# Kernel tuning notes

Measured on AMD Instinct MI355X. Metric: run time of the kernel, lower is better.

## Reference

```python
import jax, jax.numpy as jnp
import numpy as np

N = 100000        # num nodes
E = 1600000       # num edges
IN_DIM = 256
HID = 64          # per-head out_dim
OUT_DIM = 256
H = 4             # num heads
EDGE_DIM = 16
NEG_SLOPE = 0.2

def _xavier(key, shape):
    fan_in, fan_out = shape[-2], shape[-1]
    bound = float(np.sqrt(6.0 / (fan_in + fan_out)))
    return jax.random.uniform(key, shape, jnp.float32, -bound, bound)

def setup_inputs() -> dict:
    key = jax.random.key(0)
    ks = jax.random.split(key, 8)
    x = jax.random.normal(ks[0], (N, IN_DIM), jnp.float32)
    edge_index = jax.random.randint(ks[1], (2, E), 0, N, jnp.int64)
    edge_attr = jax.random.normal(ks[2], (E, EDGE_DIM), jnp.float32)
    W = _xavier(ks[3], (H, IN_DIM, HID))
    W_edge = _xavier(ks[4], (H, EDGE_DIM, HID))
    att = _xavier(ks[5], (H, 3 * HID, 1))[..., 0]          # [H, 3*HID]
    proj_w = _xavier(ks[6], (H * HID, OUT_DIM))
    proj_b = jnp.zeros((OUT_DIM,), jnp.float32)
    return {"x": x, "edge_index": edge_index, "edge_attr": edge_attr,
            "W": W, "W_edge": W_edge, "att": att,
            "proj_w": proj_w, "proj_b": proj_b}

def reference(x, edge_index, edge_attr, W, W_edge, att, proj_w, proj_b):
    src = edge_index[0]  # x_j (source) indices
    dst = edge_index[1]  # x_i (target) indices; softmax/aggregation segments

    # Per-head node transform: [H, N, HID]
    xw = jnp.einsum('ni,hio->hno', x, W)
    x_i = xw[:, dst]                                  # [H, E, HID]
    x_j = xw[:, src]                                  # [H, E, HID]
    edge_proj = jnp.einsum('ed,hdo->heo', edge_attr, W_edge)  # [H, E, HID]

    a1, a2, a3 = att[:, :HID], att[:, HID:2*HID], att[:, 2*HID:]  # [H, HID] each
    e = (jnp.einsum('heo,ho->he', x_i, a1)
         + jnp.einsum('heo,ho->he', x_j, a2)
         + jnp.einsum('heo,ho->he', edge_proj, a3))   # [H, E]
    e = jnp.where(e >= 0, e, NEG_SLOPE * e)           # LeakyReLU

    def seg_softmax(eh):  # eh: [E]
        m = jax.ops.segment_max(eh, dst, num_segments=N)
        m = jnp.where(jnp.isfinite(m), m, 0.0)
        ex = jnp.exp(eh - m[dst])
        s = jax.ops.segment_sum(ex, dst, num_segments=N)
        return ex / (s[dst] + 1e-16)

    alpha = jax.vmap(seg_softmax)(e)                  # [H, E]  (dropout: eval mode)

    msg = x_j * alpha[..., None]                      # [H, E, HID]
    out_h = jax.vmap(lambda m: jax.ops.segment_sum(m, dst, num_segments=N))(msg)  # [H, N, HID]
    out = jnp.transpose(out_h, (1, 0, 2)).reshape(N, H * HID)  # concat heads
    out = out @ proj_w + proj_b
    return jax.nn.elu(out)
```

## Files before the change

### kernel.cpp

```cpp
#include <hip/hip_runtime.h>
#include <hip/hip_bf16.h>
#include <stdint.h>

#define N_NODES 100000
#define E_EDGES 1600000
#define NEG_SLOPE 0.2f
#define NBUCK 1563
#define BK_SH 6
#define CAP 1536

typedef short short8 __attribute__((ext_vector_type(8)));
typedef float f32x4 __attribute__((ext_vector_type(4)));

__device__ __forceinline__ unsigned short f2bf(float f) {
  union { float f; unsigned int u; } c; c.f = f;
  unsigned int u = c.u;
  unsigned int r = u + 0x7FFFu + ((u >> 16) & 1u);
  return (unsigned short)(r >> 16);
}
__device__ __forceinline__ float asf(unsigned int u) {
  union { unsigned int u; float f; } c; c.u = u;
  return c.f;
}

__global__ void k_detect(const void* ei, int* flag) {
  int t = threadIdx.x;
  int v = ((const int*)ei)[2 * t + 1];
  unsigned long long b = __ballot(v != 0);
  if (t == 0) *flag = (b != 0ull) ? 1 : 0;
}

__global__ void k_prep(const float* __restrict__ W, const float* __restrict__ proj_w,
                       const float* __restrict__ W_edge, const float* __restrict__ att,
                       unsigned short* __restrict__ Bt, unsigned short* __restrict__ Pt,
                       float* __restrict__ w3) {
  int t = blockIdx.x * 256 + threadIdx.x;
  if (t < 65536) {
    int col = t >> 8, k = t & 255;
    int h = col >> 6, o = col & 63;
    Bt[t] = f2bf(W[h * 16384 + k * 64 + o]);
  } else if (t < 131072) {
    int t2 = t - 65536;
    int o = t2 >> 8, i = t2 & 255;
    int orig = (i >> 6) * 64 + ((i >> 2) & 15) + 16 * (i & 3);
    Pt[t2] = f2bf(proj_w[orig * 256 + o]);
  } else if (t < 131136) {
    int t3 = t - 131072;
    int h = t3 >> 4, d = t3 & 15;
    float s = 0.f;
    for (int o = 0; o < 64; ++o)
      s += W_edge[h * 1024 + d * 64 + o] * att[h * 192 + 128 + o];
    w3[t3] = s;
  }
}

__global__ __launch_bounds__(256, 4) void k_gemm_x(const float* __restrict__ x,
    const unsigned short* __restrict__ Bt, const float* __restrict__ att,
    unsigned int* __restrict__ xwq, float* __restrict__ scl4,
    float* __restrict__ s1, float* __restrict__ s2) {
  __shared__ unsigned short As[16384];
  const int bm = blockIdx.x * 64;
  const int t = threadIdx.x;

#pragma unroll
  for (int i = 0; i < 16; ++i) {
    int c = i * 256 + t;
    int row = c >> 6, f4 = c & 63;
    uint2 w = make_uint2(0u, 0u);
    if (bm + row < N_NODES) {
      float4 v = *(const float4*)(x + (size_t)(bm + row) * 256 + f4 * 4);
      w.x = (unsigned int)f2bf(v.x) | ((unsigned int)f2bf(v.y) << 16);
      w.y = (unsigned int)f2bf(v.z) | ((unsigned int)f2bf(v.w) << 16);
    }
    int phys = row * 512 + (((f4 >> 1) ^ (row & 7)) << 4) + ((f4 & 1) << 3);
    *(uint2*)((char*)As + phys) = w;
  }
  __syncthreads();

  const int wave = t >> 6;
  const int lane = t & 63;
  const int l16 = lane & 15, lg = lane >> 4;
  const int colbase = wave * 64;
  f32x4 acc[4][4];
#pragma unroll
  for (int i = 0; i < 4; i++)
#pragma unroll
    for (int j = 0; j < 4; j++) acc[i][j] = (f32x4){0.f, 0.f, 0.f, 0.f};

  short8 bcur[4], bnxt[4];
#pragma unroll
  for (int ni = 0; ni < 4; ni++)
    bcur[ni] = *(const short8*)(Bt + (colbase + ni * 16 + l16) * 256 + lg * 8);

#pragma unroll
  for (int ks = 0; ks < 8; ++ks) {
    short8 a[4];
#pragma unroll
    for (int mi = 0; mi < 4; mi++) {
      int row = mi * 16 + l16;
      int phys = row * 512 + (((ks * 4 + lg) ^ (row & 7)) << 4);
      a[mi] = *(const short8*)((const char*)As + phys);
    }
    if (ks < 7) {
      const int k0n = (ks + 1) * 32 + lg * 8;
#pragma unroll
      for (int ni = 0; ni < 4; ni++)
        bnxt[ni] = *(const short8*)(Bt + (colbase + ni * 16 + l16) * 256 + k0n);
    }
#pragma unroll
    for (int mi = 0; mi < 4; mi++)
#pragma unroll
      for (int ni = 0; ni < 4; ni++)
        acc[mi][ni] = __builtin_amdgcn_mfma_f32_16x16x32_bf16(a[mi], bcur[ni], acc[mi][ni], 0, 0, 0);
#pragma unroll
    for (int ni = 0; ni < 4; ni++) bcur[ni] = bnxt[ni];
  }

  float a1v[4], a2v[4];
#pragma unroll
  for (int ni = 0; ni < 4; ni++) {
    a1v[ni] = att[wave * 192 + ni * 16 + l16];
    a2v[ni] = att[wave * 192 + 64 + ni * 16 + l16];
  }
#pragma unroll
  for (int mi = 0; mi < 4; mi++) {
#pragma unroll
    for (int r = 0; r < 4; r++) {
      int row = bm + mi * 16 + lg * 4 + r;
      float a0 = acc[mi][0][r], a1 = acc[mi][1][r], a2 = acc[mi][2][r], a3 = acc[mi][3][r];
      float p1 = a0 * a1v[0] + a1 * a1v[1] + a2 * a1v[2] + a3 * a1v[3];
      float p2 = a0 * a2v[0] + a1 * a2v[1] + a2 * a2v[2] + a3 * a2v[3];
      float mx = fmaxf(fmaxf(fabsf(a0), fabsf(a1)), fmaxf(fabsf(a2), fabsf(a3)));
#pragma unroll
      for (int m = 1; m < 16; m <<= 1) {
        p1 += __shfl_xor(p1, m, 64);
        p2 += __shfl_xor(p2, m, 64);
        mx = fmaxf(mx, __shfl_xor(mx, m, 64));
      }
      if (row < N_NODES) {
        mx += 1e-30f;
        float inv = 127.f / mx;
        int q0 = __float2int_rn(a0 * inv);
        int q1 = __float2int_rn(a1 * inv);
        int q2 = __float2int_rn(a2 * inv);
        int q3 = __float2int_rn(a3 * inv);
        unsigned int pk = (q0 & 0xFF) | ((q1 & 0xFF) << 8) | ((q2 & 0xFF) << 16) |
                          ((unsigned int)(q3 & 0xFF) << 24);
        xwq[(size_t)row * 64 + wave * 16 + l16] = pk;
        if (l16 == 0) {
          s1[row * 4 + wave] = p1;
          s2[row * 4 + wave] = p2;
          scl4[row * 4 + wave] = mx * (1.f / 127.f);
        }
      }
    }
  }
}

__global__ __launch_bounds__(1024) void k_hist(const void* ei, const int* __restrict__ flag,
                                               int* __restrict__ bhist) {
  __shared__ int h[NBUCK];
  for (int i = threadIdx.x; i < NBUCK; i += 1024) h[i] = 0;
  __syncthreads();
  int f = *flag;
  int base = blockIdx.x * 4096;
#pragma unroll
  for (int k = 0; k < 4; ++k) {
    int e = base + k * 1024 + threadIdx.x;
    if (e < E_EDGES) {
      int dst = f ? ((const int*)ei)[E_EDGES + e] : (int)(((const long long*)ei)[E_EDGES + e]);
      atomicAdd(&h[dst >> BK_SH], 1);
    }
  }
  __syncthreads();
  for (int i = threadIdx.x; i < NBUCK; i += 1024) {
    int c = h[i];
    if (c) atomicAdd(&bhist[i], c);
  }
}

__global__ __launch_bounds__(1024) void k_scanb(const int* __restrict__ bhist,
                                                int* __restrict__ boff, int* __restrict__ bcur) {
  __shared__ int s[2048];
  int t = threadIdx.x;
  int ia = t, ib = t + 1024;
  int va = (ia < NBUCK) ? bhist[ia] : 0;
  int vb = (ib < NBUCK) ? bhist[ib] : 0;
  s[ia] = va; s[ib] = vb;
  __syncthreads();
  for (int off = 1; off < 2048; off <<= 1) {
    int xa = (ia >= off) ? s[ia - off] : 0;
    int xb = (ib >= off) ? s[ib - off] : 0;
    __syncthreads();
    s[ia] += xa; s[ib] += xb;
    __syncthreads();
  }
  if (ia < NBUCK) { boff[ia] = s[ia] - va; bcur[ia] = s[ia] - va; }
  if (ib < NBUCK) { boff[ib] = s[ib] - vb; bcur[ib] = s[ib] - vb; }
  if (t == 0) boff[NBUCK] = E_EDGES;
}

__global__ __launch_bounds__(1024) void k_edge(const void* ei, const int* __restrict__ flag,
                       const float* __restrict__ edge_attr,
                       const float* __restrict__ s1, const float* __restrict__ s2,
                       const float* __restrict__ w3g, int* __restrict__ bcur,
                       uint4* __restrict__ evs) {
  __shared__ float w3[64];
  __shared__ int cnt[NBUCK];
  __shared__ int rb[NBUCK];
  __shared__ int cur[NBUCK];
  const int t = threadIdx.x;
  for (int i = t; i < NBUCK; i += 1024) { cnt[i] = 0; cur[i] = 0; }
  if (t < 64) w3[t] = w3g[t];
  __syncthreads();

  const int f = *flag;
  const int base = blockIdx.x * 4096;
  int dstv[4], srcv[4];
  unsigned int pav[4], pbv[4];
#pragma unroll
  for (int k = 0; k < 4; ++k) {
    int e = base + k * 1024 + t;
    dstv[k] = -1;
    if (e < E_EDGES) {
      int src, dst;
      if (f) {
        src = ((const int*)ei)[e];
        dst = ((const int*)ei)[E_EDGES + e];
      } else {
        src = (int)(((const long long*)ei)[e]);
        dst = (int)(((const long long*)ei)[E_EDGES + e]);
      }
      float4 sd = *(const float4*)(s1 + (size_t)dst * 4);
      float4 ss = *(const float4*)(s2 + (size_t)src * 4);
      float ea[16];
#pragma unroll
      for (int i = 0; i < 4; i++) {
        float4 v = *(const float4*)(edge_attr + (size_t)e * 16 + i * 4);
        ea[4 * i] = v.x; ea[4 * i + 1] = v.y; ea[4 * i + 2] = v.z; ea[4 * i + 3] = v.w;
      }
      float ex[4];
#pragma unroll
      for (int h = 0; h < 4; h++) {
        float d = 0.f;
#pragma unroll
        for (int i = 0; i < 16; i++) d += ea[i] * w3[h * 16 + i];
        float v = (&sd.x)[h] + (&ss.x)[h] + d;
        v = (v >= 0.f) ? v : NEG_SLOPE * v;
        ex[h] = __expf(v);
      }
      dstv[k] = dst;
      srcv[k] = src;
      pav[k] = ((unsigned int)f2bf(ex[1]) << 16) | (unsigned int)f2bf(ex[0]);
      pbv[k] = ((unsigned int)f2bf(ex[3]) << 16) | (unsigned int)f2bf(ex[2]);
      atomicAdd(&cnt[dst >> BK_SH], 1);
    }
  }
  __syncthreads();
  for (int i = t; i < NBUCK; i += 1024) {
    int c = cnt[i];
    if (c) rb[i] = atomicAdd(&bcur[i], c);
  }
  __syncthreads();
#pragma unroll
  for (int k = 0; k < 4; ++k) {
    if (dstv[k] >= 0) {
      int bk = dstv[k] >> BK_SH;
      int pos = rb[bk] + atomicAdd(&cur[bk], 1);
      evs[pos] = make_uint4((unsigned int)srcv[k], pav[k], pbv[k],
                            (unsigned int)(dstv[k] & 63));
    }
  }
}

__global__ __launch_bounds__(256) void k_aggr(const int* __restrict__ boff,
    const uint4* __restrict__ evs, const unsigned int* __restrict__ xwq,
    const float* __restrict__ scl4, unsigned short* __restrict__ out_hb) {
  __shared__ int lsrc[CAP];
  __shared__ uint2 lw[CAP];
  __shared__ int cnt[64], bs[64], cur[64];
  const int b = blockIdx.x;
  const int t = threadIdx.x;
  const int e0 = boff[b];
  const int ne = boff[b + 1] - e0;
  if (t < 64) { cnt[t] = 0; cur[t] = 0; }
  __syncthreads();
  const bool ok = (ne <= CAP);
  if (ok) {
    uint4 rv[6];
#pragma unroll
    for (int k = 0; k < 6; ++k) {
      int i = k * 256 + t;
      if (i < ne) {
        rv[k] = evs[e0 + i];
        atomicAdd(&cnt[rv[k].w], 1);
      }
    }
    __syncthreads();
    if (t < 64) bs[t] = cnt[t];
    __syncthreads();
    for (int off = 1; off < 64; off <<= 1) {
      int x = 0;
      if (t < 64 && t >= off) x = bs[t - off];
      __syncthreads();
      if (t < 64) bs[t] += x;
      __syncthreads();
    }
#pragma unroll
    for (int k = 0; k < 6; ++k) {
      int i = k * 256 + t;
      if (i < ne) {
        int ld = rv[k].w;
        int slot = bs[ld] - cnt[ld] + atomicAdd(&cur[ld], 1);
        lsrc[slot] = (int)rv[k].x;
        lw[slot] = make_uint2(rv[k].y, rv[k].z);
      }
    }
    __syncthreads();
  }

  const int wv = t >> 6, lane = t & 63;
  const int hsel = lane >> 4;
  const bool hlo2 = (hsel < 2);
  const bool hodd = (hsel & 1);

#define EDGE_FMA(wv_, sc_, u_)                                            \
  {                                                                       \
    unsigned int wp = hlo2 ? (wv_).x : (wv_).y;                           \
    float wlo = asf(wp << 16), whi = asf(wp & 0xFFFF0000u);               \
    float w = hodd ? whi : wlo;                                           \
    den += w;                                                             \
    float ws = w * (sc_);                                                 \
    acc0 += ws * (float)(int)(signed char)((u_) & 0xFF);                  \
    acc1 += ws * (float)(int)(signed char)(((u_) >> 8) & 0xFF);           \
    acc2 += ws * (float)(int)(signed char)(((u_) >> 16) & 0xFF);          \
    acc3 += ws * (float)(int)(signed char)((u_) >> 24);                   \
  }

  for (int r = 0; r < 16; ++r) {
    const int ln = wv * 16 + r;
    const int n = b * 64 + ln;
    if (n >= N_NODES) break;
    float acc0 = 0.f, acc1 = 0.f, acc2 = 0.f, acc3 = 0.f, den = 0.f;
    if (ok) {
      const int je = bs[ln];
      int j = je - cnt[ln];
      for (; j + 4 <= je; j += 4) {
        int s0 = lsrc[j], s1_ = lsrc[j + 1], s2_ = lsrc[j + 2], s3_ = lsrc[j + 3];
        uint2 w0 = lw[j], w1 = lw[j + 1], w2 = lw[j + 2], w3_ = lw[j + 3];
        float c0 = scl4[(size_t)s0 * 4 + hsel];
        float c1 = scl4[(size_t)s1_ * 4 + hsel];
        float c2 = scl4[(size_t)s2_ * 4 + hsel];
        float c3 = scl4[(size_t)s3_ * 4 + hsel];
        unsigned int u0 = xwq[(size_t)s0 * 64 + lane];
        unsigned int u1 = xwq[(size_t)s1_ * 64 + lane];
        unsigned int u2 = xwq[(size_t)s2_ * 64 + lane];
        unsigned int u3 = xwq[(size_t)s3_ * 64 + lane];
        EDGE_FMA(w0, c0, u0);
        EDGE_FMA(w1, c1, u1);
        EDGE_FMA(w2, c2, u2);
        EDGE_FMA(w3_, c3, u3);
      }
      for (; j < je; ++j) {
        int s0 = lsrc[j];
        uint2 w0 = lw[j];
        float c0 = scl4[(size_t)s0 * 4 + hsel];
        unsigned int u0 = xwq[(size_t)s0 * 64 + lane];
        EDGE_FMA(w0, c0, u0);
      }
    } else {
      for (int i = 0; i < ne; ++i) {
        uint4 v0 = evs[e0 + i];
        if ((int)v0.w == ln) {
          uint2 w0 = make_uint2(v0.y, v0.z);
          float c0 = scl4[(size_t)v0.x * 4 + hsel];
          unsigned int u0 = xwq[(size_t)v0.x * 64 + lane];
          EDGE_FMA(w0, c0, u0);
        }
      }
    }
    float d = den + 1e-16f;
    uint2 o;
    o.x = ((unsigned int)f2bf(acc1 / d) << 16) | (unsigned int)f2bf(acc0 / d);
    o.y = ((unsigned int)f2bf(acc3 / d) << 16) | (unsigned int)f2bf(acc2 / d);
    *(uint2*)(out_hb + (size_t)n * 256 + lane * 4) = o;
  }
#undef EDGE_FMA
}

__global__ __launch_bounds__(256, 4) void k_gemm_out(const unsigned short* __restrict__ A,
    const unsigned short* __restrict__ Pt, const float* __restrict__ bias,
    float* __restrict__ out) {
  __shared__ __align__(16) char smem[32768];
  unsigned short* As = (unsigned short*)smem;
  float* Ls = (float*)smem;
  const int bm = blockIdx.x * 64;
  const int t = threadIdx.x;

#pragma unroll
  for (int i = 0; i < 8; ++i) {
    int c = i * 256 + t;
    int row = c >> 5, G = c & 31;
    short8 v = (short8){0, 0, 0, 0, 0, 0, 0, 0};
    if (bm + row < N_NODES) v = *(const short8*)(A + (size_t)(bm + row) * 256 + G * 8);
    int phys = row * 512 + ((G ^ (row & 7)) << 4);
    *(short8*)((char*)As + phys) = v;
  }
  __syncthreads();

  const int wave = t >> 6;
  const int lane = t & 63;
  const int l16 = lane & 15, lg = lane >> 4;
  const int colbase = wave * 64;
  f32x4 acc[4][4];
#pragma unroll
  for (int i = 0; i < 4; i++)
#pragma unroll
    for (int j = 0; j < 4; j++) acc[i][j] = (f32x4){0.f, 0.f, 0.f, 0.f};

  short8 bcur[4], bnxt[4];
#pragma unroll
  for (int ni = 0; ni < 4; ni++)
    bcur[ni] = *(const short8*)(Pt + (colbase + ni * 16 + l16) * 256 + lg * 8);

#pragma unroll
  for (int ks = 0; ks < 8; ++ks) {
    short8 a[4];
#pragma unroll
    for (int mi = 0; mi < 4; mi++) {
      int row = mi * 16 + l16;
      int phys = row * 512 + (((ks * 4 + lg) ^ (row & 7)) << 4);
      a[mi] = *(const short8*)((const char*)As + phys);
    }
    if (ks < 7) {
      const int k0n = (ks + 1) * 32 + lg * 8;
#pragma unroll
      for (int ni = 0; ni < 4; ni++)
        bnxt[ni] = *(const short8*)(Pt + (colbase + ni * 16 + l16) * 256 + k0n);
    }
#pragma unroll
    for (int mi = 0; mi < 4; mi++)
#pragma unroll
      for (int ni = 0; ni < 4; ni++)
        acc[mi][ni] = __builtin_amdgcn_mfma_f32_16x16x32_bf16(a[mi], bcur[ni], acc[mi][ni], 0, 0, 0);
#pragma unroll
    for (int ni = 0; ni < 4; ni++) bcur[ni] = bnxt[ni];
  }

  const int row16 = t >> 4;
  const int q = t & 15;
#pragma unroll
  for (int mi = 0; mi < 4; mi++) {
    __syncthreads();
#pragma unroll
    for (int r = 0; r < 4; r++) {
#pragma unroll
      for (int ni = 0; ni < 4; ni++)
        Ls[(lg * 4 + r) * 260 + colbase + ni * 16 + l16] = acc[mi][ni][r];
    }
    __syncthreads();
    int grow = bm + mi * 16 + row16;
    if (grow < N_NODES) {
#pragma unroll
      for (int k = 0; k < 4; ++k) {
        int qc = (q + k * 16) * 4;
        float4 v = *(const float4*)&Ls[row16 * 260 + qc];
        float4 bv = *(const float4*)(bias + qc);
        v.x += bv.x; v.y += bv.y; v.z += bv.z; v.w += bv.w;
        v.x = (v.x > 0.f) ? v.x : (__expf(v.x) - 1.f);
        v.y = (v.y > 0.f) ? v.y : (__expf(v.y) - 1.f);
        v.z = (v.z > 0.f) ? v.z : (__expf(v.z) - 1.f);
        v.w = (v.w > 0.f) ? v.w : (__expf(v.w) - 1.f);
        *(float4*)(out + (size_t)grow * 256 + qc) = v;
      }
    }
  }
}

extern "C" void kernel_launch(void* const* d_in, const int* in_sizes, int n_in,
                              void* d_out, int out_size, void* d_ws, size_t ws_size,
                              hipStream_t stream) {
  const float* x = (const float*)d_in[0];
  const void* ei = d_in[1];
  const float* edge_attr = (const float*)d_in[2];
  const float* W = (const float*)d_in[3];
  const float* W_edge = (const float*)d_in[4];
  const float* att = (const float*)d_in[5];
  const float* proj_w = (const float*)d_in[6];
  const float* proj_b = (const float*)d_in[7];
  float* out = (float*)d_out;

  char* ws = (char*)d_ws;
  size_t off = 0;
  auto alloc = [&](size_t bytes) -> void* {
    void* p = (void*)(ws + off);
    off += (bytes + 255) & ~(size_t)255;
    return p;
  };
  unsigned int* xwq     = (unsigned int*)alloc((size_t)N_NODES * 256);
  float* scl4    = (float*)alloc((size_t)N_NODES * 4 * 4);
  unsigned short* outhb = (unsigned short*)alloc((size_t)N_NODES * 256 * 2);
  float* s1      = (float*)alloc((size_t)N_NODES * 4 * 4);
  float* s2      = (float*)alloc((size_t)N_NODES * 4 * 4);
  uint4* evs     = (uint4*)alloc((size_t)E_EDGES * 16);
  int* bhist     = (int*)alloc((size_t)NBUCK * 4);
  int* boff      = (int*)alloc((size_t)(NBUCK + 1) * 4);
  int* bcur      = (int*)alloc((size_t)NBUCK * 4);
  unsigned short* Bt = (unsigned short*)alloc(65536 * 2);
  unsigned short* Pt = (unsigned short*)alloc(65536 * 2);
  float* w3      = (float*)alloc(64 * 4);
  int* flag      = (int*)alloc(256);

  const int NB_E = (E_EDGES + 4095) / 4096;

  hipMemsetAsync(bhist, 0, (size_t)NBUCK * 4, stream);
  k_detect<<<1, 64, 0, stream>>>(ei, flag);
  k_prep<<<(131136 + 255) / 256, 256, 0, stream>>>(W, proj_w, W_edge, att, Bt, Pt, w3);
  k_gemm_x<<<(N_NODES + 63) / 64, 256, 0, stream>>>(x, Bt, att, xwq, scl4, s1, s2);
  k_hist<<<NB_E, 1024, 0, stream>>>(ei, flag, bhist);
  k_scanb<<<1, 1024, 0, stream>>>(bhist, boff, bcur);
  k_edge<<<NB_E, 1024, 0, stream>>>(ei, flag, edge_attr, s1, s2, w3, bcur, evs);
  k_aggr<<<NBUCK, 256, 0, stream>>>(boff, evs, xwq, scl4, outhb);
  k_gemm_out<<<(N_NODES + 63) / 64, 256, 0, stream>>>(outhb, Pt, proj_b, out);
}
```

Before: 310.6 us.

## Stage GEMM epilogue through LDS to emit contiguous int8 rows with vector stores

The GEMM epilogue now writes each 16-row accumulator slice into shared memory and reads it back so that each thread owns 16 contiguous columns of one row. Quantization, the attention dot products and the abs-max reduction then run per thread, each thread writes 16 bytes of packed int8 with one store, and only two shuffle steps are needed instead of four. This changes the element order in xwq to plain column order, so the proj_w permutation in prep is dropped to match. The cost is extra LDS traffic and barriers per slice, plus a larger shared-memory footprint that may lower occupancy.

```diff
diff --git a/kernel.cpp b/kernel.cpp
--- a/kernel.cpp
+++ b/kernel.cpp
@@ -42,8 +42,7 @@
   } else if (t < 131072) {
     int t2 = t - 65536;
     int o = t2 >> 8, i = t2 & 255;
-    int orig = (i >> 6) * 64 + ((i >> 2) & 15) + 16 * (i & 3);
-    Pt[t2] = f2bf(proj_w[orig * 256 + o]);
+    Pt[t2] = f2bf(proj_w[i * 256 + o]);
   } else if (t < 131136) {
     int t3 = t - 131072;
     int h = t3 >> 4, d = t3 & 15;
@@ -58,7 +57,10 @@
     const unsigned short* __restrict__ Bt, const float* __restrict__ att,
     unsigned int* __restrict__ xwq, float* __restrict__ scl4,
     float* __restrict__ s1, float* __restrict__ s2) {
-  __shared__ unsigned short As[16384];
+  __shared__ __align__(16) char smem[32768];
+  unsigned short* As = (unsigned short*)smem;
+  float* Ls = (float*)smem;
+  float* attS = (float*)(smem + 24576);
   const int bm = blockIdx.x * 64;
   const int t = threadIdx.x;
 
@@ -116,42 +118,59 @@
     for (int ni = 0; ni < 4; ni++) bcur[ni] = bnxt[ni];
   }
 
-  float a1v[4], a2v[4];
-#pragma unroll
-  for (int ni = 0; ni < 4; ni++) {
-    a1v[ni] = att[wave * 192 + ni * 16 + l16];
-    a2v[ni] = att[wave * 192 + 64 + ni * 16 + l16];
-  }
+  __syncthreads();
+  for (int i = t; i < 768; i += 256) attS[i] = att[i];
+
+  const int row16 = t >> 4;
+  const int g = t & 15;
+  const int h = g >> 2;
+  const int cwh = (g & 3) * 16;
 #pragma unroll
   for (int mi = 0; mi < 4; mi++) {
-#pragma unroll
-    for (int r = 0; r < 4; r++) {
-      int row = bm + mi * 16 + lg * 4 + r;
-      float a0 = acc[mi][0][r], a1 = acc[mi][1][r], a2 = acc[mi][2][r], a3 = acc[mi][3][r];
-      float p1 = a0 * a1v[0] + a1 * a1v[1] + a2 * a1v[2] + a3 * a1v[3];
-      float p2 = a0 * a2v[0] + a1 * a2v[1] + a2 * a2v[2] + a3 * a2v[3];
-      float mx = fmaxf(fmaxf(fabsf(a0), fabsf(a1)), fmaxf(fabsf(a2), fabsf(a3)));
-#pragma unroll
-      for (int m = 1; m < 16; m <<= 1) {
-        p1 += __shfl_xor(p1, m, 64);
-        p2 += __shfl_xor(p2, m, 64);
-        mx = fmaxf(mx, __shfl_xor(mx, m, 64));
-      }
-      if (row < N_NODES) {
-        mx += 1e-30f;
-        float inv = 127.f / mx;
-        int q0 = __float2int_rn(a0 * inv);
-        int q1 = __float2int_rn(a1 * inv);
-        int q2 = __float2int_rn(a2 * inv);
-        int q3 = __float2int_rn(a3 * inv);
-        unsigned int pk = (q0 & 0xFF) | ((q1 & 0xFF) << 8) | ((q2 & 0xFF) << 16) |
-                          ((unsigned int)(q3 & 0xFF) << 24);
-        xwq[(size_t)row * 64 + wave * 16 + l16] = pk;
-        if (l16 == 0) {
-          s1[row * 4 + wave] = p1;
-          s2[row * 4 + wave] = p2;
-          scl4[row * 4 + wave] = mx * (1.f / 127.f);
-        }
+    __syncthreads();
+#pragma unroll
+    for (int r = 0; r < 4; r++)
+#pragma unroll
+      for (int ni = 0; ni < 4; ni++)
+        Ls[(lg * 4 + r) * 260 + colbase + ni * 16 + l16] = acc[mi][ni][r];
+    __syncthreads();
+    float v[16];
+#pragma unroll
+    for (int k = 0; k < 4; ++k) {
+      float4 f = *(const float4*)&Ls[row16 * 260 + g * 16 + k * 4];
+      v[4 * k] = f.x; v[4 * k + 1] = f.y; v[4 * k + 2] = f.z; v[4 * k + 3] = f.w;
+    }
+    float mx = 0.f, p1 = 0.f, p2 = 0.f;
+#pragma unroll
+    for (int j = 0; j < 16; ++j) {
+      mx = fmaxf(mx, fabsf(v[j]));
+      p1 += v[j] * attS[h * 192 + cwh + j];
+      p2 += v[j] * attS[h * 192 + 64 + cwh + j];
+    }
+    mx = fmaxf(mx, __shfl_xor(mx, 1, 64));
+    mx = fmaxf(mx, __shfl_xor(mx, 2, 64));
+    p1 += __shfl_xor(p1, 1, 64); p1 += __shfl_xor(p1, 2, 64);
+    p2 += __shfl_xor(p2, 1, 64); p2 += __shfl_xor(p2, 2, 64);
+    int row = bm + mi * 16 + row16;
+    if (row < N_NODES) {
+      mx += 1e-30f;
+      float inv = 127.f / mx;
+      uint4 pk;
+      unsigned int* pw = &pk.x;
+#pragma unroll
+      for (int k = 0; k < 4; ++k) {
+        int q0 = __float2int_rn(v[4 * k] * inv);
+        int q1 = __float2int_rn(v[4 * k + 1] * inv);
+        int q2 = __float2int_rn(v[4 * k + 2] * inv);
+        int q3 = __float2int_rn(v[4 * k + 3] * inv);
+        pw[k] = (q0 & 0xFF) | ((q1 & 0xFF) << 8) | ((q2 & 0xFF) << 16) |
+                ((unsigned int)(q3 & 0xFF) << 24);
+      }
+      *(uint4*)(xwq + (size_t)row * 64 + g * 4) = pk;
+      if ((g & 3) == 0) {
+        scl4[row * 4 + h] = mx * (1.f / 127.f);
+        s1[row * 4 + h] = p1;
+        s2[row * 4 + h] = p2;
       }
     }
   }
```

Measured after the change: 300.2 us. 1.03x faster.
